# Kernel optimization log

Hardware: AMD Instinct MI355X
Metric: run time of the kernel (lower is better)

Reference implementation:

```python
import jax, jax.numpy as jnp
import numpy as np

NUM_EMBEDDINGS = 1024
EMBEDDING_DIM = 64


def setup_inputs() -> dict:
    key = jax.random.key(0)
    k1, k2 = jax.random.split(key)
    z = jax.random.normal(k1, (64, 32, 32, EMBEDDING_DIM), dtype=jnp.float32)
    # torch init: uniform_(-1/num_embeddings, 1/num_embeddings)
    lim = 1.0 / NUM_EMBEDDINGS
    codebook = jax.random.uniform(
        k2, (NUM_EMBEDDINGS, EMBEDDING_DIM), dtype=jnp.float32,
        minval=-lim, maxval=lim)
    return {"z": z, "codebook": codebook}


def reference(z, codebook):
    # z: [..., D]; codebook: [K, D]
    z_flat = z.reshape(-1, z.shape[-1])                      # [N, D]
    # ||z||^2 - 2 z.e + ||e||^2  -> [N, K]
    distances = (
        jnp.sum(z_flat ** 2, axis=1, keepdims=True)
        - 2.0 * jnp.einsum("nd,kd->nk", z_flat, codebook)
        + jnp.sum(codebook ** 2, axis=1)
    )
    min_indices = jnp.argmin(distances, axis=1)              # [N]
    z_q = jnp.take(codebook, min_indices, axis=0).reshape(z.shape)
    return z_q, min_indices
```

## Files before the change

kernel.cpp:

```cpp
#include <hip/hip_runtime.h>
#include <hip/hip_bf16.h>
#include <math.h>


#define D      64
#define K      1024
#define BLOCK  256

typedef _Float16 half8_t __attribute__((ext_vector_type(8)));
typedef float    floatx4 __attribute__((ext_vector_type(4)));
typedef unsigned int uint4v __attribute__((ext_vector_type(4)));

#define WS_CN_OFF    0
#define WS_EF_OFF    4096

__device__ __forceinline__ float np_sumsq64_p(const float* __restrict__ x) {
    float r[8];
    {
        float4 v0 = *(const float4*)(x);
        float4 v1 = *(const float4*)(x + 4);
        r[0] = __fmul_rn(v0.x, v0.x); r[1] = __fmul_rn(v0.y, v0.y);
        r[2] = __fmul_rn(v0.z, v0.z); r[3] = __fmul_rn(v0.w, v0.w);
        r[4] = __fmul_rn(v1.x, v1.x); r[5] = __fmul_rn(v1.y, v1.y);
        r[6] = __fmul_rn(v1.z, v1.z); r[7] = __fmul_rn(v1.w, v1.w);
    }
#pragma unroll
    for (int i = 8; i < 64; i += 8) {
        float4 v0 = *(const float4*)(x + i);
        float4 v1 = *(const float4*)(x + i + 4);
        r[0] = __fadd_rn(r[0], __fmul_rn(v0.x, v0.x));
        r[1] = __fadd_rn(r[1], __fmul_rn(v0.y, v0.y));
        r[2] = __fadd_rn(r[2], __fmul_rn(v0.z, v0.z));
        r[3] = __fadd_rn(r[3], __fmul_rn(v0.w, v0.w));
        r[4] = __fadd_rn(r[4], __fmul_rn(v1.x, v1.x));
        r[5] = __fadd_rn(r[5], __fmul_rn(v1.y, v1.y));
        r[6] = __fadd_rn(r[6], __fmul_rn(v1.z, v1.z));
        r[7] = __fadd_rn(r[7], __fmul_rn(v1.w, v1.w));
    }
    return __fadd_rn(__fadd_rn(__fadd_rn(r[0], r[1]), __fadd_rn(r[2], r[3])),
                     __fadd_rn(__fadd_rn(r[4], r[5]), __fadd_rn(r[6], r[7])));
}

__device__ __forceinline__ void nt_store16(_Float16* p, half8_t v) {
    uint4v u;
    __builtin_memcpy(&u, &v, 16);
    __builtin_nontemporal_store(u, (uint4v*)p);
}

__global__ void vq_pre(const float* __restrict__ cb, float* __restrict__ cn,
                       _Float16* __restrict__ ef) {
    const int k = blockIdx.x * 64 + threadIdx.x;
    if (k < K) {
        __builtin_nontemporal_store(np_sumsq64_p(cb + (long)k * D), &cn[k]);
        const int t = k >> 6, ct = (k >> 4) & 3, l16 = k & 15;
#pragma unroll
        for (int ch = 0; ch < 2; ++ch)
#pragma unroll
            for (int quad = 0; quad < 4; ++quad) {
                const float* p = cb + (long)k * D + ch * 32 + quad * 8;
                half8_t h1, h2;
#pragma unroll
                for (int j = 0; j < 8; ++j) {
                    float x10 = __fmul_rn(p[j], 1024.0f);
                    _Float16 g1 = (_Float16)x10;
                    h1[j] = g1;
                    h2[j] = (_Float16)(__fmul_rn(__fsub_rn(x10, (float)g1), 2048.0f));
                }
                const int base = t * 8192 + ct * 2048 + 128 * quad + 8 * l16;
                nt_store16(ef + base + 512 * (ch), h1);
                nt_store16(ef + base + 512 * (2 + ch), h2);
            }
    }
    __threadfence_system();
}

__global__ __launch_bounds__(BLOCK, 2) void vq_main(
    const float* __restrict__ z, const float* __restrict__ cb,
    const _Float16* __restrict__ ef, const float* __restrict__ cn,
    float* __restrict__ zq, float* __restrict__ idx_out) {
    __shared__ __align__(16) float zf[128 * 68];
    __shared__ float sS[128];
    __shared__ float sCn[K];
    __shared__ int   sBi[128];

    const int tid  = threadIdx.x;
    const int lane = tid & 63;
    const int wv   = tid >> 6;
    const int quad = lane >> 4;
    const int l16  = lane & 15;
    const long rowbase = (long)blockIdx.x * 128;

    const float4* gz = (const float4*)(z + rowbase * D);
#pragma unroll
    for (int i = 0; i < 8; ++i) {
        int idx4 = i * BLOCK + tid;
        int r = idx4 >> 4, j = idx4 & 15;
        *(float4*)(zf + r * 68 + j * 4) = gz[idx4];
    }
#pragma unroll
    for (int i = 0; i < 4; ++i) sCn[i * 256 + tid] = cn[i * 256 + tid];
    __syncthreads();

    if (tid < 128) sS[tid] = np_sumsq64_p(zf + tid * 68);

    half8_t a1[2][2], a2[2][2];
#pragma unroll
    for (int rt = 0; rt < 2; ++rt) {
        const int row = wv * 32 + rt * 16 + l16;
#pragma unroll
        for (int ch = 0; ch < 2; ++ch) {
            const float* p = zf + row * 68 + ch * 32 + quad * 8;
            float4 f0 = *(const float4*)(p);
            float4 f1 = *(const float4*)(p + 4);
            float xs[8] = {f0.x, f0.y, f0.z, f0.w, f1.x, f1.y, f1.z, f1.w};
#pragma unroll
            for (int j = 0; j < 8; ++j) {
                _Float16 h1 = (_Float16)xs[j];
                a1[rt][ch][j] = h1;
                a2[rt][ch][j] =
                    (_Float16)(__fmul_rn(__fsub_rn(xs[j], (float)h1), 2048.0f));
            }
        }
    }
    __syncthreads();

    float myS[2][4];
#pragma unroll
    for (int rt = 0; rt < 2; ++rt)
#pragma unroll
        for (int r = 0; r < 4; ++r)
            myS[rt][r] = sS[wv * 32 + rt * 16 + quad * 4 + r];

    float bv[2][4];
    int   bi[2][4];
#pragma unroll
    for (int rt = 0; rt < 2; ++rt)
#pragma unroll
        for (int r = 0; r < 4; ++r) { bv[rt][r] = INFINITY; bi[rt][r] = 0; }

    const char* eb = (const char*)ef + 16 * lane;
    const floatx4 Z4g = {0.f, 0.f, 0.f, 0.f};

#define LOADG(b1_, b2_, cnv_, g_) do {                                        \
        const char* p_ = eb + (size_t)(g_) * 4096;                            \
        b1_[0] = *(const half8_t*)(p_);                                       \
        b1_[1] = *(const half8_t*)(p_ + 1024);                                \
        b2_[0] = *(const half8_t*)(p_ + 2048);                                \
        b2_[1] = *(const half8_t*)(p_ + 3072);                                \
        cnv_   = sCn[(g_) * 16 + l16];                                        \
    } while (0)

#define COMPUTE(b1_, b2_, cnv_, g_) do {                                      \
        const int kg_ = (g_) * 16 + l16;                                      \
        floatx4 aM0, aM1, aC0, aC1;                                           \
        aM0 = __builtin_amdgcn_mfma_f32_16x16x32_f16(a1[0][0], b1_[0], Z4g, 0, 0, 0); \
        aM1 = __builtin_amdgcn_mfma_f32_16x16x32_f16(a1[1][0], b1_[0], Z4g, 0, 0, 0); \
        aM0 = __builtin_amdgcn_mfma_f32_16x16x32_f16(a1[0][1], b1_[1], aM0, 0, 0, 0); \
        aM1 = __builtin_amdgcn_mfma_f32_16x16x32_f16(a1[1][1], b1_[1], aM1, 0, 0, 0); \
        aC0 = __builtin_amdgcn_mfma_f32_16x16x32_f16(a1[0][0], b2_[0], Z4g, 0, 0, 0); \
        aC1 = __builtin_amdgcn_mfma_f32_16x16x32_f16(a1[1][0], b2_[0], Z4g, 0, 0, 0); \
        aC0 = __builtin_amdgcn_mfma_f32_16x16x32_f16(a1[0][1], b2_[1], aC0, 0, 0, 0); \
        aC1 = __builtin_amdgcn_mfma_f32_16x16x32_f16(a1[1][1], b2_[1], aC1, 0, 0, 0); \
        aC0 = __builtin_amdgcn_mfma_f32_16x16x32_f16(a2[0][0], b1_[0], aC0, 0, 0, 0); \
        aC1 = __builtin_amdgcn_mfma_f32_16x16x32_f16(a2[1][0], b1_[0], aC1, 0, 0, 0); \
        aC0 = __builtin_amdgcn_mfma_f32_16x16x32_f16(a2[0][1], b1_[1], aC0, 0, 0, 0); \
        aC1 = __builtin_amdgcn_mfma_f32_16x16x32_f16(a2[1][1], b1_[1], aC1, 0, 0, 0); \
        _Pragma("unroll")                                                     \
        for (int r = 0; r < 4; ++r) {                                         \
            float ds0 = fmaf(aC0[r], 0x1p-11f, aM0[r]);                       \
            float d0  = __fadd_rn(__fsub_rn(myS[0][r],                        \
                            __fmul_rn(ds0, 0x1p-9f)), cnv_);                  \
            if (d0 < bv[0][r]) { bv[0][r] = d0; bi[0][r] = kg_; }             \
            float ds1 = fmaf(aC1[r], 0x1p-11f, aM1[r]);                       \
            float d1  = __fadd_rn(__fsub_rn(myS[1][r],                        \
                            __fmul_rn(ds1, 0x1p-9f)), cnv_);                  \
            if (d1 < bv[1][r]) { bv[1][r] = d1; bi[1][r] = kg_; }             \
        }                                                                     \
    } while (0)

    half8_t b1A[2], b2A[2], b1B[2], b2B[2], b1C[2], b2C[2];
    float cnvA, cnvB, cnvC;
    LOADG(b1A, b2A, cnvA, 0);
    LOADG(b1B, b2B, cnvB, 1);
    for (int g = 0; g < 63; g += 3) {
        LOADG(b1C, b2C, cnvC, g + 2);
        COMPUTE(b1A, b2A, cnvA, g);
        if (g + 3 < 64) LOADG(b1A, b2A, cnvA, g + 3);
        COMPUTE(b1B, b2B, cnvB, g + 1);
        if (g + 4 < 64) LOADG(b1B, b2B, cnvB, g + 4);
        COMPUTE(b1C, b2C, cnvC, g + 2);
    }
    COMPUTE(b1A, b2A, cnvA, 63);

#undef LOADG
#undef COMPUTE

#pragma unroll
    for (int rt = 0; rt < 2; ++rt)
#pragma unroll
        for (int r = 0; r < 4; ++r) {
            float v = bv[rt][r];
            int   x = bi[rt][r];
#pragma unroll
            for (int off = 1; off <= 8; off <<= 1) {
                float ov = __shfl_xor(v, off);
                int   ox = __shfl_xor(x, off);
                if (ov < v || (ov == v && ox < x)) { v = ov; x = ox; }
            }
            if (l16 == 0) {
                const int rl = wv * 32 + rt * 16 + quad * 4 + r;
                sBi[rl] = x;
                idx_out[rowbase + rl] = (float)x;
            }
        }
    __syncthreads();

    const float4* cb4 = (const float4*)cb;
    float4* zq4 = (float4*)(zq + rowbase * D);
#pragma unroll
    for (int i = 0; i < 8; ++i) {
        int idx4 = i * BLOCK + tid;
        int r = idx4 >> 4, j = idx4 & 15;
        zq4[idx4] = cb4[(long)sBi[r] * 16 + j];
    }
}

extern "C" void kernel_launch(void* const* d_in, const int* in_sizes, int n_in,
                              void* d_out, int out_size, void* d_ws, size_t ws_size,
                              hipStream_t stream) {
    const float* z  = (const float*)d_in[0];
    const float* cb = (const float*)d_in[1];

    const int n_rows = in_sizes[0] / D;
    float* zq      = (float*)d_out;
    float* idx_out = zq + (long)n_rows * D;

    float*    ws_cn = (float*)((char*)d_ws + WS_CN_OFF);
    _Float16* ws_ef = (_Float16*)((char*)d_ws + WS_EF_OFF);

    vq_pre<<<K / 64, 64, 0, stream>>>(cb, ws_cn, ws_ef);
    vq_main<<<n_rows / 128, BLOCK, 0, stream>>>(z, cb, ws_ef, ws_cn, zq, idx_out);
}
```

Baseline: 105.5 us.

## Pipeline codebook loads four deep with inline asm and explicit vmcnt waits

Replaces the compiler-scheduled triple-buffered codebook loads with inline-asm global_load_dwordx4 instructions, four groups in flight. Explicit s_waitcnt vmcnt waits plus sched barriers let each MFMA group start once only its own loads have landed, instead of the conservative waits the compiler inserts. This aims to hide global load latency behind MFMA work. It costs more VGPRs, which may lower occupancy, and the hand-counted vmcnt values are fragile if the compiler emits other vector memory ops.

Measured after the change: 101.6 us. -3.7%, faster.

```diff
diff --git a/kernel.cpp b/kernel.cpp
--- a/kernel.cpp
+++ b/kernel.cpp
@@ -141,13 +141,21 @@
     const char* eb = (const char*)ef + 16 * lane;
     const floatx4 Z4g = {0.f, 0.f, 0.f, 0.f};
 
-#define LOADG(b1_, b2_, cnv_, g_) do {                                        \
+#define GLD4(b1_, b2_, cnv_, g_) do {                                         \
         const char* p_ = eb + (size_t)(g_) * 4096;                            \
-        b1_[0] = *(const half8_t*)(p_);                                       \
-        b1_[1] = *(const half8_t*)(p_ + 1024);                                \
-        b2_[0] = *(const half8_t*)(p_ + 2048);                                \
-        b2_[1] = *(const half8_t*)(p_ + 3072);                                \
-        cnv_   = sCn[(g_) * 16 + l16];                                        \
+        asm volatile(                                                         \
+            "global_load_dwordx4 %0, %4, off\n\t"                             \
+            "global_load_dwordx4 %1, %4, off offset:1024\n\t"                 \
+            "global_load_dwordx4 %2, %4, off offset:2048\n\t"                 \
+            "global_load_dwordx4 %3, %4, off offset:3072"                     \
+            : "=&v"(b1_[0]), "=&v"(b1_[1]), "=&v"(b2_[0]), "=&v"(b2_[1])      \
+            : "v"(p_));                                                       \
+        cnv_ = sCn[(g_) * 16 + l16];                                          \
+    } while (0)
+
+#define VWAIT(N_) do {                                                        \
+        asm volatile("s_waitcnt vmcnt(" N_ ")");                              \
+        __builtin_amdgcn_sched_barrier(0);                                    \
     } while (0)
 
 #define COMPUTE(b1_, b2_, cnv_, g_) do {                                      \
@@ -178,21 +186,37 @@
         }                                                                     \
     } while (0)
 
-    half8_t b1A[2], b2A[2], b1B[2], b2B[2], b1C[2], b2C[2];
-    float cnvA, cnvB, cnvC;
-    LOADG(b1A, b2A, cnvA, 0);
-    LOADG(b1B, b2B, cnvB, 1);
-    for (int g = 0; g < 63; g += 3) {
-        LOADG(b1C, b2C, cnvC, g + 2);
+    half8_t b1A[2], b2A[2], b1B[2], b2B[2], b1C[2], b2C[2], b1D[2], b2D[2];
+    float cnvA, cnvB, cnvC, cnvD;
+    GLD4(b1A, b2A, cnvA, 0);
+    GLD4(b1B, b2B, cnvB, 1);
+    GLD4(b1C, b2C, cnvC, 2);
+    for (int g = 0; g < 60; g += 4) {
+        GLD4(b1D, b2D, cnvD, g + 3);
+        VWAIT("12");
         COMPUTE(b1A, b2A, cnvA, g);
-        if (g + 3 < 64) LOADG(b1A, b2A, cnvA, g + 3);
+        GLD4(b1A, b2A, cnvA, g + 4);
+        VWAIT("12");
         COMPUTE(b1B, b2B, cnvB, g + 1);
-        if (g + 4 < 64) LOADG(b1B, b2B, cnvB, g + 4);
+        GLD4(b1B, b2B, cnvB, g + 5);
+        VWAIT("12");
         COMPUTE(b1C, b2C, cnvC, g + 2);
-    }
-    COMPUTE(b1A, b2A, cnvA, 63);
-
-#undef LOADG
+        GLD4(b1C, b2C, cnvC, g + 6);
+        VWAIT("12");
+        COMPUTE(b1D, b2D, cnvD, g + 3);
+    }
+    GLD4(b1D, b2D, cnvD, 63);
+    VWAIT("12");
+    COMPUTE(b1A, b2A, cnvA, 60);
+    VWAIT("8");
+    COMPUTE(b1B, b2B, cnvB, 61);
+    VWAIT("4");
+    COMPUTE(b1C, b2C, cnvC, 62);
+    VWAIT("0");
+    COMPUTE(b1D, b2D, cnvD, 63);
+
+#undef GLD4
+#undef VWAIT
 #undef COMPUTE
 
 #pragma unroll
```
